# Optimization experiments

Measured on AMD Instinct MI355X. Metric: run time of the kernel, lower is better.

The kernel has to match this reference:

```python
import jax, jax.numpy as jnp
import numpy as np

B, A, L, M, E = 4096, 64, 16, 4, 10
K = (4, 16, 32)
Q = (2, 4, 6)
P = (32, 128, 256)


def setup_inputs() -> dict:
    key = jax.random.key(0)
    ks = iter(jax.random.split(key, 32))
    inp = {}
    inp['x'] = jax.random.normal(next(ks), (B, A, L, M), dtype=jnp.float32)
    inp['y'] = jax.random.uniform(next(ks), (B, E), dtype=jnp.float32)
    inp['w1'] = jax.random.normal(next(ks), (E, K[0], Q[0], A), dtype=jnp.float32) / (K[0] * Q[0])
    inp['w2'] = jax.random.normal(next(ks), (E, K[1], Q[1], A), dtype=jnp.float32) / (K[1] * Q[1])
    inp['w3'] = jax.random.normal(next(ks), (E, K[2], Q[2], A), dtype=jnp.float32) / (K[2] * Q[2])
    inp['coeff1'] = jax.random.normal(next(ks), (P[0],), dtype=jnp.float32)
    inp['coeff2'] = jax.random.normal(next(ks), (P[1],), dtype=jnp.float32)
    inp['coeff3'] = jax.random.normal(next(ks), (P[2],), dtype=jnp.float32)
    ri = lambda n, hi: jax.random.randint(next(ks), (n,), 0, hi, dtype=jnp.int32)
    inp['i1'] = ri(P[0], L); inp['l1'] = ri(P[0], M)
    inp['k1'] = ri(P[0], K[0]); inp['q1'] = ri(P[0], Q[0])
    inp['i2'] = ri(P[1], L); inp['j2'] = ri(P[1], L)
    inp['l2'] = ri(P[1], M); inp['m2'] = ri(P[1], M)
    inp['k2'] = ri(P[1], K[1]); inp['q2'] = ri(P[1], Q[1])
    inp['i3'] = ri(P[2], L); inp['j3'] = ri(P[2], L); inp['f3'] = ri(P[2], L)
    inp['l3'] = ri(P[2], M); inp['m3'] = ri(P[2], M); inp['g3'] = ri(P[2], M)
    inp['k3'] = ri(P[2], K[2]); inp['q3'] = ri(P[2], Q[2])
    return inp


def _forward(x, y, w1, w2, w3, coeff1, coeff2, coeff3,
             i1, l1, k1, q1,
             i2, j2, l2, m2, k2, q2,
             i3, j3, f3, l3, m3, g3, k3, q3):
    # element-mixed weights: [B, K, Q, A]
    wy1 = jnp.einsum('ekqa,be->bkqa', w1, y)
    wy2 = jnp.einsum('ekqa,be->bkqa', w2, y)
    wy3 = jnp.einsum('ekqa,be->bkqa', w3, y)
    # sparse path contraction (equivalent to dense 'ik,lq,ekqa,bail,be->ba' etc.)
    g1 = jnp.transpose(wy1[:, k1, q1, :], (0, 2, 1))          # [B, A, P1]
    t1 = jnp.einsum('bap,p->ba', x[:, :, i1, l1] * g1, coeff1)
    g2 = jnp.transpose(wy2[:, k2, q2, :], (0, 2, 1))          # [B, A, P2]
    t2 = jnp.einsum('bap,p->ba', x[:, :, i2, l2] * x[:, :, j2, m2] * g2, coeff2)
    g3_ = jnp.transpose(wy3[:, k3, q3, :], (0, 2, 1))         # [B, A, P3]
    t3 = jnp.einsum('bap,p->ba',
                    x[:, :, i3, l3] * x[:, :, j3, m3] * x[:, :, f3, g3] * g3_,
                    coeff3)
    return t1 + t2 + t3  # [B, A] (scalar irrep_out -> flattened view)


def reference(x, y, w1, w2, w3, coeff1, coeff2, coeff3,
              i1, l1, k1, q1,
              i2, j2, l2, m2, k2, q2,
              i3, j3, f3, l3, m3, g3, k3, q3):
    return _forward(x, y, w1, w2, w3, coeff1, coeff2, coeff3,
                    i1, l1, k1, q1,
                    i2, j2, l2, m2, k2, q2,
                    i3, j3, f3, l3, m3, g3, k3, q3)
```

## Files before the change

kernel.cpp:

```cpp
#include <hip/hip_runtime.h>
#include <hip/hip_bf16.h>

typedef _Float16 f16x8 __attribute__((ext_vector_type(8)));
typedef _Float16 f16x4 __attribute__((ext_vector_type(4)));
typedef float    f32x4 __attribute__((ext_vector_type(4)));

constexpr int BB  = 4096;
constexpr int AA  = 64;
constexpr int ED  = 10;
constexpr int P1N = 32, P2N = 128, P3N = 256;
constexpr int PT  = 416;
constexpr int NKS = 13;
constexpr int KSPL = 7;
constexpr int BCH = 32;
constexpr int NCH = 4;

__global__ void build_idx_kernel(
    const int* __restrict__ i1, const int* __restrict__ l1,
    const int* __restrict__ i2, const int* __restrict__ j2,
    const int* __restrict__ l2, const int* __restrict__ m2,
    const int* __restrict__ i3, const int* __restrict__ j3,
    const int* __restrict__ f3, const int* __restrict__ l3,
    const int* __restrict__ m3, const int* __restrict__ g3,
    unsigned* __restrict__ idxs) {
  const int p = threadIdx.x;
  if (p >= PT) return;
  unsigned sa, sb = 64, sc = 64;
  if (p < P1N) {
    sa = i1[p] * 4 + l1[p];
  } else if (p < P1N + P2N) {
    int pp = p - P1N;
    sa = i2[pp] * 4 + l2[pp];
    sb = j2[pp] * 4 + m2[pp];
  } else {
    int pp = p - P1N - P2N;
    sa = i3[pp] * 4 + l3[pp];
    sb = j3[pp] * 4 + m3[pp];
    sc = f3[pp] * 4 + g3[pp];
  }
  idxs[p] = (sa * 8) | ((sb * 8) << 10) | ((sc * 8) << 20);
}

__global__ void build_cwb_kernel(
    const float* __restrict__ w1, const float* __restrict__ w2, const float* __restrict__ w3,
    const float* __restrict__ c1, const float* __restrict__ c2, const float* __restrict__ c3,
    const int* __restrict__ k1, const int* __restrict__ q1,
    const int* __restrict__ k2, const int* __restrict__ q2,
    const int* __restrict__ k3, const int* __restrict__ q3,
    _Float16* __restrict__ cwb) {
  const int a  = blockIdx.x & 63;
  const int ks = blockIdx.x >> 6;
  const int l  = threadIdx.x;
  const int grp = l >> 4, e = l & 15;
  _Float16* dst = cwb + (((size_t)a * NKS + ks) * 64 + l) * 8;
  #pragma unroll
  for (int j = 0; j < 8; ++j) {
    const int p = ks * 32 + grp * 8 + j;
    float v = 0.f;
    if (e < ED) {
      const float* w; float coeff; int k, q, K, Q;
      if (p < P1N)            { w = w1; coeff = c1[p]; k = k1[p]; q = q1[p]; K = 4;  Q = 2; }
      else if (p < P1N + P2N) { int pp = p - P1N;       w = w2; coeff = c2[pp]; k = k2[pp]; q = q2[pp]; K = 16; Q = 4; }
      else                    { int pp = p - P1N - P2N; w = w3; coeff = c3[pp]; k = k3[pp]; q = q3[pp]; K = 32; Q = 6; }
      v = coeff * w[(((size_t)e * K + k) * Q + q) * AA + a];
    }
    dst[j] = (_Float16)v;
  }
}

__global__ __launch_bounds__(256, 4)
void contract_kernel(const float* __restrict__ x, const float* __restrict__ y,
                     const unsigned* __restrict__ idxs,
                     const f16x8* __restrict__ cwb,
                     float* __restrict__ out) {
  __shared__ f16x4 xls[BCH][65];
  __shared__ float yls[BCH][17];

  const int t  = threadIdx.x;
  const int a0 = (blockIdx.x & 15) * NCH;
  const int b0 = (blockIdx.x >> 4) * BCH;

  for (int u = t; u < BCH * 64; u += 256) {
    const int b = u >> 6, s = u & 63;
    const float* xb = x + (size_t)(b0 + b) * 4096 + a0 * 64 + s;
    f16x4 v;
    v[0] = (_Float16)xb[0];
    v[1] = (_Float16)xb[64];
    v[2] = (_Float16)xb[128];
    v[3] = (_Float16)xb[192];
    xls[b][s] = v;
  }
  if (t < BCH) {
    f16x4 one;
    one[0] = one[1] = one[2] = one[3] = (_Float16)1.0f;
    xls[t][64] = one;
    const float* yb = y + (size_t)(b0 + t) * ED;
    #pragma unroll
    for (int e = 0; e < ED; ++e) yls[t][e] = yb[e];
    #pragma unroll
    for (int e = ED; e < 16; ++e) yls[t][e] = 0.f;
  }
  __syncthreads();

  const int wv = t >> 6, l = t & 63, grp = l >> 4, er = l & 15;
  const int mt = wv & 1;
  const int kh = wv >> 1;
  const char* __restrict__ rowb = (const char*)&xls[mt * 16 + er][0];
  const f16x8* __restrict__ cw0 = cwb + ((size_t)(a0 + 0) * NKS) * 64 + l;
  const f16x8* __restrict__ cw1 = cwb + ((size_t)(a0 + 1) * NKS) * 64 + l;
  const f16x8* __restrict__ cw2 = cwb + ((size_t)(a0 + 2) * NKS) * 64 + l;
  const f16x8* __restrict__ cw3 = cwb + ((size_t)(a0 + 3) * NKS) * 64 + l;
  const uint4*  __restrict__ ip  = (const uint4*)idxs + grp * 2;

  f32x4 ac0 = {0.f, 0.f, 0.f, 0.f};
  f32x4 ac1 = {0.f, 0.f, 0.f, 0.f};
  f32x4 ac2 = {0.f, 0.f, 0.f, 0.f};
  f32x4 ac3 = {0.f, 0.f, 0.f, 0.f};

  const int ks_beg = kh ? KSPL : 0;
  const int ks_end = kh ? NKS : KSPL;

  for (int ks = ks_beg; ks < ks_end; ++ks) {
    const uint4 iA = ip[ks * 8 + 0];
    const uint4 iB = ip[ks * 8 + 1];
    const f16x8 b0f = cw0[ks * 64];
    const f16x8 b1f = cw1[ks * 64];
    const f16x8 b2f = cw2[ks * 64];
    const f16x8 b3f = cw3[ks * 64];
    const unsigned pks[8] = {iA.x, iA.y, iA.z, iA.w, iB.x, iB.y, iB.z, iB.w};

    f16x4 g0[8], g1[8], g2[8];
    #pragma unroll
    for (int j = 0; j < 8; ++j) {
      const unsigned pk = pks[j];
      g0[j] = *(const f16x4*)(rowb + (pk & 1023u));
      g1[j] = *(const f16x4*)(rowb + ((pk >> 10) & 1023u));
      g2[j] = *(const f16x4*)(rowb + (pk >> 20));
    }

    f16x8 af0, af1, af2, af3;
    #pragma unroll
    for (int j = 0; j < 8; ++j) {
      const f16x4 v = g0[j] * g1[j] * g2[j];
      af0[j] = v[0]; af1[j] = v[1]; af2[j] = v[2]; af3[j] = v[3];
    }

    ac0 = __builtin_amdgcn_mfma_f32_16x16x32_f16(af0, b0f, ac0, 0, 0, 0);
    ac1 = __builtin_amdgcn_mfma_f32_16x16x32_f16(af1, b1f, ac1, 0, 0, 0);
    ac2 = __builtin_amdgcn_mfma_f32_16x16x32_f16(af2, b2f, ac2, 0, 0, 0);
    ac3 = __builtin_amdgcn_mfma_f32_16x16x32_f16(af3, b3f, ac3, 0, 0, 0);
  }

  __syncthreads();
  float* scr = (float*)&xls[0][0];
  const int sbase = (mt * 64 + l) * 17;
  if (kh == 1) {
    #pragma unroll
    for (int v = 0; v < 4; ++v) {
      scr[sbase + v + 0]  = ac0[v];
      scr[sbase + v + 4]  = ac1[v];
      scr[sbase + v + 8]  = ac2[v];
      scr[sbase + v + 12] = ac3[v];
    }
  }
  __syncthreads();
  if (kh == 0) {
    #pragma unroll
    for (int v = 0; v < 4; ++v) {
      ac0[v] += scr[sbase + v + 0];
      ac1[v] += scr[sbase + v + 4];
      ac2[v] += scr[sbase + v + 8];
      ac3[v] += scr[sbase + v + 12];
    }
    #pragma unroll
    for (int c = 0; c < NCH; ++c) {
      const f32x4 acc = c == 0 ? ac0 : c == 1 ? ac1 : c == 2 ? ac2 : ac3;
      float s0 = acc[0] * yls[mt * 16 + grp * 4 + 0][er];
      float s1 = acc[1] * yls[mt * 16 + grp * 4 + 1][er];
      float s2 = acc[2] * yls[mt * 16 + grp * 4 + 2][er];
      float s3 = acc[3] * yls[mt * 16 + grp * 4 + 3][er];
      #pragma unroll
      for (int m = 1; m < 16; m <<= 1) {
        s0 += __shfl_xor(s0, m);
        s1 += __shfl_xor(s1, m);
        s2 += __shfl_xor(s2, m);
        s3 += __shfl_xor(s3, m);
      }
      if (er < 4) {
        const float sv = er == 0 ? s0 : er == 1 ? s1 : er == 2 ? s2 : s3;
        out[(size_t)(b0 + mt * 16 + grp * 4 + er) * AA + (a0 + c)] = sv;
      }
    }
  }
}

extern "C" void kernel_launch(void* const* d_in, const int* in_sizes, int n_in,
                              void* d_out, int out_size, void* d_ws, size_t ws_size,
                              hipStream_t stream) {
  const float* x  = (const float*)d_in[0];
  const float* y  = (const float*)d_in[1];
  const float* w1 = (const float*)d_in[2];
  const float* w2 = (const float*)d_in[3];
  const float* w3 = (const float*)d_in[4];
  const float* c1 = (const float*)d_in[5];
  const float* c2 = (const float*)d_in[6];
  const float* c3 = (const float*)d_in[7];
  const int* i1 = (const int*)d_in[8];
  const int* l1 = (const int*)d_in[9];
  const int* k1 = (const int*)d_in[10];
  const int* q1 = (const int*)d_in[11];
  const int* i2 = (const int*)d_in[12];
  const int* j2 = (const int*)d_in[13];
  const int* l2 = (const int*)d_in[14];
  const int* m2 = (const int*)d_in[15];
  const int* k2 = (const int*)d_in[16];
  const int* q2 = (const int*)d_in[17];
  const int* i3 = (const int*)d_in[18];
  const int* j3 = (const int*)d_in[19];
  const int* f3 = (const int*)d_in[20];
  const int* l3 = (const int*)d_in[21];
  const int* m3 = (const int*)d_in[22];
  const int* g3 = (const int*)d_in[23];
  const int* k3 = (const int*)d_in[24];
  const int* q3 = (const int*)d_in[25];

  unsigned*  idxs = (unsigned*)d_ws;
  _Float16*  cwb  = (_Float16*)((char*)d_ws + 4096);

  build_idx_kernel<<<1, 448, 0, stream>>>(i1, l1, i2, j2, l2, m2,
                                          i3, j3, f3, l3, m3, g3, idxs);
  build_cwb_kernel<<<AA * NKS, 64, 0, stream>>>(w1, w2, w3, c1, c2, c3,
                                                k1, q1, k2, q2, k3, q3, cwb);
  contract_kernel<<<(AA / NCH) * (BB / BCH), 256, 0, stream>>>(
      x, y, idxs, (const f16x8*)cwb, (float*)d_out);
}
```

Before: 42.81 us.

## Split batch across waves, fully unroll K-steps with factor-count specialization and prefetch

Each wave now owns its own 16 batch rows (BCH raised to 64) and walks all 13 K-steps, replacing the old split-K across wave pairs and the shared-memory cross-wave reduction with its extra barriers. The K loop is fully unrolled through a template that skips the multiplies and LDS gathers by the constant x=1 factor for order-1 and order-2 path segments. The next step's indices and weight fragments are also prefetched in registers. In exchange there are half as many blocks, and more LDS per block (64 rows of x), which may lower occupancy. Each wave also carries a longer serial chain.

Result: faster. 40.23 us (-6.0%).

```diff
diff --git a/kernel.cpp b/kernel.cpp
--- a/kernel.cpp
+++ b/kernel.cpp
@@ -11,8 +11,7 @@
 constexpr int P1N = 32, P2N = 128, P3N = 256;
 constexpr int PT  = 416;
 constexpr int NKS = 13;
-constexpr int KSPL = 7;
-constexpr int BCH = 32;
+constexpr int BCH = 64;
 constexpr int NCH = 4;
 
 __global__ void build_idx_kernel(
@@ -68,6 +67,51 @@
   }
 }
 
+template <int NF, int KS, bool LAST>
+__device__ __forceinline__ void kstep(
+    const char* __restrict__ rowb, const uint4* __restrict__ ip,
+    const f16x8* __restrict__ cw0, const f16x8* __restrict__ cw1,
+    const f16x8* __restrict__ cw2, const f16x8* __restrict__ cw3,
+    uint4 iA, uint4 iB,
+    f16x8 b0, f16x8 b1, f16x8 b2, f16x8 b3,
+    uint4& nA, uint4& nB,
+    f16x8& n0, f16x8& n1, f16x8& n2, f16x8& n3,
+    f32x4& ac0, f32x4& ac1, f32x4& ac2, f32x4& ac3) {
+  if constexpr (!LAST) {
+    nA = ip[(KS + 1) * 8];
+    nB = ip[(KS + 1) * 8 + 1];
+    n0 = cw0[(KS + 1) * 64];
+    n1 = cw1[(KS + 1) * 64];
+    n2 = cw2[(KS + 1) * 64];
+    n3 = cw3[(KS + 1) * 64];
+  }
+  const unsigned pks[8] = {iA.x, iA.y, iA.z, iA.w, iB.x, iB.y, iB.z, iB.w};
+  f16x8 af0, af1, af2, af3;
+  #pragma unroll
+  for (int jh = 0; jh < 2; ++jh) {
+    f16x4 g0[4], g1[4], g2[4];
+    #pragma unroll
+    for (int j = 0; j < 4; ++j) {
+      const unsigned pk = pks[jh * 4 + j];
+      g0[j] = *(const f16x4*)(rowb + (pk & 1023u));
+      if (NF >= 2) g1[j] = *(const f16x4*)(rowb + ((pk >> 10) & 1023u));
+      if (NF >= 3) g2[j] = *(const f16x4*)(rowb + (pk >> 20));
+    }
+    #pragma unroll
+    for (int j = 0; j < 4; ++j) {
+      f16x4 v = g0[j];
+      if (NF >= 2) v = v * g1[j];
+      if (NF >= 3) v = v * g2[j];
+      const int jj = jh * 4 + j;
+      af0[jj] = v[0]; af1[jj] = v[1]; af2[jj] = v[2]; af3[jj] = v[3];
+    }
+  }
+  ac0 = __builtin_amdgcn_mfma_f32_16x16x32_f16(af0, b0, ac0, 0, 0, 0);
+  ac1 = __builtin_amdgcn_mfma_f32_16x16x32_f16(af1, b1, ac1, 0, 0, 0);
+  ac2 = __builtin_amdgcn_mfma_f32_16x16x32_f16(af2, b2, ac2, 0, 0, 0);
+  ac3 = __builtin_amdgcn_mfma_f32_16x16x32_f16(af3, b3, ac3, 0, 0, 0);
+}
+
 __global__ __launch_bounds__(256, 4)
 void contract_kernel(const float* __restrict__ x, const float* __restrict__ y,
                      const unsigned* __restrict__ idxs,
@@ -103,9 +147,7 @@
   __syncthreads();
 
   const int wv = t >> 6, l = t & 63, grp = l >> 4, er = l & 15;
-  const int mt = wv & 1;
-  const int kh = wv >> 1;
-  const char* __restrict__ rowb = (const char*)&xls[mt * 16 + er][0];
+  const char* __restrict__ rowb = (const char*)&xls[wv * 16 + er][0];
   const f16x8* __restrict__ cw0 = cwb + ((size_t)(a0 + 0) * NKS) * 64 + l;
   const f16x8* __restrict__ cw1 = cwb + ((size_t)(a0 + 1) * NKS) * 64 + l;
   const f16x8* __restrict__ cw2 = cwb + ((size_t)(a0 + 2) * NKS) * 64 + l;
@@ -117,79 +159,38 @@
   f32x4 ac2 = {0.f, 0.f, 0.f, 0.f};
   f32x4 ac3 = {0.f, 0.f, 0.f, 0.f};
 
-  const int ks_beg = kh ? KSPL : 0;
-  const int ks_end = kh ? NKS : KSPL;
-
-  for (int ks = ks_beg; ks < ks_end; ++ks) {
-    const uint4 iA = ip[ks * 8 + 0];
-    const uint4 iB = ip[ks * 8 + 1];
-    const f16x8 b0f = cw0[ks * 64];
-    const f16x8 b1f = cw1[ks * 64];
-    const f16x8 b2f = cw2[ks * 64];
-    const f16x8 b3f = cw3[ks * 64];
-    const unsigned pks[8] = {iA.x, iA.y, iA.z, iA.w, iB.x, iB.y, iB.z, iB.w};
-
-    f16x4 g0[8], g1[8], g2[8];
-    #pragma unroll
-    for (int j = 0; j < 8; ++j) {
-      const unsigned pk = pks[j];
-      g0[j] = *(const f16x4*)(rowb + (pk & 1023u));
-      g1[j] = *(const f16x4*)(rowb + ((pk >> 10) & 1023u));
-      g2[j] = *(const f16x4*)(rowb + (pk >> 20));
-    }
-
-    f16x8 af0, af1, af2, af3;
-    #pragma unroll
-    for (int j = 0; j < 8; ++j) {
-      const f16x4 v = g0[j] * g1[j] * g2[j];
-      af0[j] = v[0]; af1[j] = v[1]; af2[j] = v[2]; af3[j] = v[3];
-    }
-
-    ac0 = __builtin_amdgcn_mfma_f32_16x16x32_f16(af0, b0f, ac0, 0, 0, 0);
-    ac1 = __builtin_amdgcn_mfma_f32_16x16x32_f16(af1, b1f, ac1, 0, 0, 0);
-    ac2 = __builtin_amdgcn_mfma_f32_16x16x32_f16(af2, b2f, ac2, 0, 0, 0);
-    ac3 = __builtin_amdgcn_mfma_f32_16x16x32_f16(af3, b3f, ac3, 0, 0, 0);
-  }
-
-  __syncthreads();
-  float* scr = (float*)&xls[0][0];
-  const int sbase = (mt * 64 + l) * 17;
-  if (kh == 1) {
-    #pragma unroll
-    for (int v = 0; v < 4; ++v) {
-      scr[sbase + v + 0]  = ac0[v];
-      scr[sbase + v + 4]  = ac1[v];
-      scr[sbase + v + 8]  = ac2[v];
-      scr[sbase + v + 12] = ac3[v];
-    }
-  }
-  __syncthreads();
-  if (kh == 0) {
-    #pragma unroll
-    for (int v = 0; v < 4; ++v) {
-      ac0[v] += scr[sbase + v + 0];
-      ac1[v] += scr[sbase + v + 4];
-      ac2[v] += scr[sbase + v + 8];
-      ac3[v] += scr[sbase + v + 12];
-    }
-    #pragma unroll
-    for (int c = 0; c < NCH; ++c) {
-      const f32x4 acc = c == 0 ? ac0 : c == 1 ? ac1 : c == 2 ? ac2 : ac3;
-      float s0 = acc[0] * yls[mt * 16 + grp * 4 + 0][er];
-      float s1 = acc[1] * yls[mt * 16 + grp * 4 + 1][er];
-      float s2 = acc[2] * yls[mt * 16 + grp * 4 + 2][er];
-      float s3 = acc[3] * yls[mt * 16 + grp * 4 + 3][er];
-      #pragma unroll
-      for (int m = 1; m < 16; m <<= 1) {
-        s0 += __shfl_xor(s0, m);
-        s1 += __shfl_xor(s1, m);
-        s2 += __shfl_xor(s2, m);
-        s3 += __shfl_xor(s3, m);
-      }
-      if (er < 4) {
-        const float sv = er == 0 ? s0 : er == 1 ? s1 : er == 2 ? s2 : s3;
-        out[(size_t)(b0 + mt * 16 + grp * 4 + er) * AA + (a0 + c)] = sv;
-      }
+  uint4 cA = ip[0], cB = ip[1];
+  f16x8 cb0 = cw0[0], cb1 = cw1[0], cb2 = cw2[0], cb3 = cw3[0];
+
+  #define STEP(NF, KS, LAST)                                                  \
+    kstep<NF, KS, LAST>(rowb, ip, cw0, cw1, cw2, cw3, cA, cB,                 \
+                        cb0, cb1, cb2, cb3, cA, cB, cb0, cb1, cb2, cb3,       \
+                        ac0, ac1, ac2, ac3)
+  STEP(1, 0, false);
+  STEP(2, 1, false); STEP(2, 2, false);
+  STEP(2, 3, false); STEP(2, 4, false);
+  STEP(3, 5, false); STEP(3, 6, false); STEP(3, 7, false);
+  STEP(3, 8, false); STEP(3, 9, false); STEP(3, 10, false);
+  STEP(3, 11, false); STEP(3, 12, true);
+  #undef STEP
+
+  #pragma unroll
+  for (int c = 0; c < NCH; ++c) {
+    const f32x4 acc = c == 0 ? ac0 : c == 1 ? ac1 : c == 2 ? ac2 : ac3;
+    float s0 = acc[0] * yls[wv * 16 + grp * 4 + 0][er];
+    float s1 = acc[1] * yls[wv * 16 + grp * 4 + 1][er];
+    float s2 = acc[2] * yls[wv * 16 + grp * 4 + 2][er];
+    float s3 = acc[3] * yls[wv * 16 + grp * 4 + 3][er];
+    #pragma unroll
+    for (int m = 1; m < 16; m <<= 1) {
+      s0 += __shfl_xor(s0, m);
+      s1 += __shfl_xor(s1, m);
+      s2 += __shfl_xor(s2, m);
+      s3 += __shfl_xor(s3, m);
+    }
+    if (er < 4) {
+      const float sv = er == 0 ? s0 : er == 1 ? s1 : er == 2 ? s2 : s3;
+      out[(size_t)(b0 + wv * 16 + grp * 4 + er) * AA + (a0 + c)] = sv;
     }
   }
 }
```
